# Performance work log

Hardware: AMD Instinct MI355X
Metric: run time of the kernel (lower is better)

The kernel has to match this reference:

```python
import jax, jax.numpy as jnp
import numpy as np


def setup_inputs() -> dict:
    key = jax.random.key(0)
    k1, k2 = jax.random.split(key)
    reconstructed_image = jax.random.normal(k1, (8, 1, 256, 256), dtype=jnp.float32)
    mask_embedding = jax.random.normal(k2, (8, 32, 256, 256), dtype=jnp.float32)
    return {"reconstructed_image": reconstructed_image, "mask_embedding": mask_embedding}


def reference(reconstructed_image, mask_embedding):
    # Original module: K = ortho-normalized 2D FFT of the real image;
    # for each k-space column i, zero all other columns, take ortho ifft2,
    # keep the real part -> separate_images[b, i, h, w].
    # By FFT linearity, ifft2 of a single-column k-space factorizes:
    #   ifft2(M_i * K)[h, w] = ifft_height(K[:, i])[h] * exp(2j*pi*w*i/W) / sqrt(W)
    # so we never materialize the (B, W, 2, H, W) masked k-space tensor.
    img = reconstructed_image[:, 0]                      # (B, H, W) real
    B, H, W = img.shape
    K = jnp.fft.fft2(img, norm='ortho')                  # (B, H, W) complex64
    col = jnp.fft.ifft(K, axis=1, norm='ortho')          # ifft along height: col[b, h, i]
    w_idx = jnp.arange(W)
    # phase[i, w] = exp(2j*pi*i*w/W) / sqrt(W)  (analytic width-basis)
    phase = (jnp.exp(2j * jnp.pi * jnp.outer(w_idx, w_idx) / W) / np.float32(np.sqrt(W))).astype(jnp.complex64)
    # separate_images[b, i, h, w] = Re(col[b, h, i] * phase[i, w])
    sep = jnp.einsum('bhi,iw->bihw', col, phase).real.astype(reconstructed_image.dtype)
    return jnp.concatenate([sep, mask_embedding], axis=1)  # (B, W+E, H, W)
```

## Files before the change

kernel.cpp:

```cpp
#include <hip/hip_runtime.h>


#define TWO_PI_OVER_256 0.02454369260617026f

typedef float vfloat4 __attribute__((ext_vector_type(4)));

__global__ __launch_bounds__(256) void dft_rows_kernel(const float* __restrict__ img,
                                                       float2* __restrict__ Ct) {
    __shared__ float row[256];
    const int t  = threadIdx.x;
    const int bh = blockIdx.x;
    row[t] = img[(size_t)bh * 256 + t];

    float ci, si;
    __sincosf((float)t * TWO_PI_OVER_256, &si, &ci);
    __syncthreads();

    float re = 0.f, im = 0.f;
    for (int xo = 0; xo < 256; xo += 32) {
        const int k = (t * xo) & 255;
        float c, s;
        __sincosf((float)k * TWO_PI_OVER_256, &s, &c);
#pragma unroll
        for (int x2 = 0; x2 < 32; ++x2) {
            const float r = row[xo + x2];
            re = fmaf(r, c, re);
            im = fmaf(r, s, im);
            const float cn = fmaf(c, ci, -s * si);
            s = fmaf(s, ci, c * si);
            c = cn;
        }
    }
    const int b = bh >> 8;
    const int h = bh & 255;
    Ct[((size_t)(b * 256 + t)) * 256 + h] =
        make_float2(re * (1.f / 256.f), im * (-1.f / 256.f));
}

__global__ __launch_bounds__(256) void expand_kernel(const float2* __restrict__ Ct,
                                                     float* __restrict__ out) {
    const int t   = threadIdx.x;
    const int blk = blockIdx.x;
    const int b   = blk >> 8;
    const int i   = blk & 255;

    __shared__ float2 cp[256];
    cp[t] = Ct[(size_t)blk * 256 + t];

    const int wb = (t & 63) * 4;
    float cw[4], sw[4];
#pragma unroll
    for (int j = 0; j < 4; ++j) {
        const int k = (i * (wb + j)) & 255;
        __sincosf((float)k * TWO_PI_OVER_256, &sw[j], &cw[j]);
    }
    __syncthreads();

    const int hl = t >> 6;
    float* __restrict__ obase = out + ((size_t)b * 288 + i) * 65536;
#pragma unroll 4
    for (int it = 0; it < 64; ++it) {
        const int h = it * 4 + hl;
        const float2 cv = cp[h];
        vfloat4 v;
        v.x = cv.x * cw[0] - cv.y * sw[0];
        v.y = cv.x * cw[1] - cv.y * sw[1];
        v.z = cv.x * cw[2] - cv.y * sw[2];
        v.w = cv.x * cw[3] - cv.y * sw[3];
        __builtin_nontemporal_store(v, reinterpret_cast<vfloat4*>(obase + (size_t)h * 256 + wb));
    }
}

__global__ __launch_bounds__(256) void mask_copy_kernel(const vfloat4* __restrict__ m,
                                                        vfloat4* __restrict__ out) {
    const size_t e = (size_t)blockIdx.x * 256 + threadIdx.x;
    const size_t b = e >> 19;
    const size_t r = e & 524287;
    const vfloat4 v = __builtin_nontemporal_load(&m[b * 524288 + r]);
    __builtin_nontemporal_store(v, &out[b * 4718592 + 4194304 + r]);
}

extern "C" void kernel_launch(void* const* d_in, const int* in_sizes, int n_in,
                              void* d_out, int out_size, void* d_ws, size_t ws_size,
                              hipStream_t stream) {
    const float* img  = (const float*)d_in[0];
    const float* mask = (const float*)d_in[1];
    float* out = (float*)d_out;

    float2* Ct = (float2*)(out + (size_t)256 * 65536);

    dft_rows_kernel<<<2048, 256, 0, stream>>>(img, Ct);
    expand_kernel<<<2048, 256, 0, stream>>>(Ct, out);
    mask_copy_kernel<<<16384, 256, 0, stream>>>((const vfloat4*)mask, (vfloat4*)out);
}
```

Measured before the change: 650.8 us.

## Fuse row DFT, expansion and mask copy into one kernel

Merges the three launches into a single kernel. Blocks past 2048 copy the mask embedding, eight vectors per thread. The other blocks compute, for their column i, the row DFT of each image row tile in shared memory, reduced with lane shuffles, and then write the expanded outputs directly. This removes the intermediate Ct buffer round trip and two launches, but each of the 256 blocks per batch now recomputes its own column's DFT over the whole image, reading it repeatedly from cache.

```diff
diff --git a/kernel.cpp b/kernel.cpp
--- a/kernel.cpp
+++ b/kernel.cpp
@@ -2,82 +2,95 @@
 
 
 #define TWO_PI_OVER_256 0.02454369260617026f
+#define SR 260
 
 typedef float vfloat4 __attribute__((ext_vector_type(4)));
 
-__global__ __launch_bounds__(256) void dft_rows_kernel(const float* __restrict__ img,
-                                                       float2* __restrict__ Ct) {
-    __shared__ float row[256];
-    const int t  = threadIdx.x;
-    const int bh = blockIdx.x;
-    row[t] = img[(size_t)bh * 256 + t];
-
-    float ci, si;
-    __sincosf((float)t * TWO_PI_OVER_256, &si, &ci);
-    __syncthreads();
-
-    float re = 0.f, im = 0.f;
-    for (int xo = 0; xo < 256; xo += 32) {
-        const int k = (t * xo) & 255;
-        float c, s;
-        __sincosf((float)k * TWO_PI_OVER_256, &s, &c);
-#pragma unroll
-        for (int x2 = 0; x2 < 32; ++x2) {
-            const float r = row[xo + x2];
-            re = fmaf(r, c, re);
-            im = fmaf(r, s, im);
-            const float cn = fmaf(c, ci, -s * si);
-            s = fmaf(s, ci, c * si);
-            c = cn;
-        }
-    }
-    const int b = bh >> 8;
-    const int h = bh & 255;
-    Ct[((size_t)(b * 256 + t)) * 256 + h] =
-        make_float2(re * (1.f / 256.f), im * (-1.f / 256.f));
-}
-
-__global__ __launch_bounds__(256) void expand_kernel(const float2* __restrict__ Ct,
-                                                     float* __restrict__ out) {
+__global__ __launch_bounds__(256) void fused_kernel(const float* __restrict__ img,
+                                                    const vfloat4* __restrict__ mask,
+                                                    float* __restrict__ out) {
     const int t   = threadIdx.x;
     const int blk = blockIdx.x;
-    const int b   = blk >> 8;
-    const int i   = blk & 255;
 
-    __shared__ float2 cp[256];
-    cp[t] = Ct[(size_t)blk * 256 + t];
+    if (blk >= 2048) {
+        const int mb = blk - 2048;
+#pragma unroll
+        for (int k = 0; k < 8; ++k) {
+            const size_t e = (size_t)mb * 256 + t + (size_t)k * 524288;
+            const size_t b = e >> 19;
+            const size_t r = e & 524287;
+            const vfloat4 v = __builtin_nontemporal_load(&mask[b * 524288 + r]);
+            __builtin_nontemporal_store(v, (vfloat4*)out + b * 4718592 + 4194304 + r);
+        }
+        return;
+    }
 
-    const int wb = (t & 63) * 4;
+    __shared__ float  rows[32 * SR];
+    __shared__ float2 cp[32];
+    const int b = blk >> 8;
+    const int i = blk & 255;
+
+    const int xc = t & 7;
+    const int hl = t >> 3;
+    float c0, s0, cst, sst;
+    __sincosf((float)((i * xc) & 255) * TWO_PI_OVER_256, &s0, &c0);
+    __sincosf((float)((i * 8)  & 255) * TWO_PI_OVER_256, &sst, &cst);
+
+    const int wb  = (t & 63) * 4;
+    const int hl2 = t >> 6;
     float cw[4], sw[4];
 #pragma unroll
     for (int j = 0; j < 4; ++j) {
         const int k = (i * (wb + j)) & 255;
         __sincosf((float)k * TWO_PI_OVER_256, &sw[j], &cw[j]);
     }
-    __syncthreads();
 
-    const int hl = t >> 6;
-    float* __restrict__ obase = out + ((size_t)b * 288 + i) * 65536;
-#pragma unroll 4
-    for (int it = 0; it < 64; ++it) {
-        const int h = it * 4 + hl;
-        const float2 cv = cp[h];
-        vfloat4 v;
-        v.x = cv.x * cw[0] - cv.y * sw[0];
-        v.y = cv.x * cw[1] - cv.y * sw[1];
-        v.z = cv.x * cw[2] - cv.y * sw[2];
-        v.w = cv.x * cw[3] - cv.y * sw[3];
-        __builtin_nontemporal_store(v, reinterpret_cast<vfloat4*>(obase + (size_t)h * 256 + wb));
+    const float* __restrict__ imgb  = img + (size_t)b * 65536;
+    float* __restrict__       obase = out + ((size_t)b * 288 + i) * 65536;
+
+    for (int tile = 0; tile < 8; ++tile) {
+        const int h0 = tile * 32;
+        const float2* __restrict__ src = (const float2*)(imgb + h0 * 256);
+#pragma unroll
+        for (int j = 0; j < 8; ++j) {
+            const int idx = t + j * 256;
+            const int rr  = idx >> 7;
+            const int c2  = idx & 127;
+            *(float2*)&rows[rr * SR + 2 * c2]        = src[rr * 128 + c2];
+            *(float2*)&rows[(rr + 16) * SR + 2 * c2] = src[(rr + 16) * 128 + c2];
+        }
+        __syncthreads();
+
+        float re = 0.f, im = 0.f, c = c0, s = s0;
+        const float* __restrict__ rp = &rows[hl * SR + xc];
+#pragma unroll
+        for (int x2 = 0; x2 < 32; ++x2) {
+            const float rv = rp[8 * x2];
+            re = fmaf(rv, c, re);
+            im = fmaf(rv, s, im);
+            const float cn = fmaf(c, cst, -s * sst);
+            s = fmaf(s, cst, c * sst);
+            c = cn;
+        }
+        re += __shfl_xor(re, 1); im += __shfl_xor(im, 1);
+        re += __shfl_xor(re, 2); im += __shfl_xor(im, 2);
+        re += __shfl_xor(re, 4); im += __shfl_xor(im, 4);
+        if (xc == 0) cp[hl] = make_float2(re * (1.f / 256.f), im * (-1.f / 256.f));
+        __syncthreads();
+
+#pragma unroll
+        for (int it2 = 0; it2 < 8; ++it2) {
+            const int h = it2 * 4 + hl2;
+            const float2 cv = cp[h];
+            vfloat4 v;
+            v.x = cv.x * cw[0] - cv.y * sw[0];
+            v.y = cv.x * cw[1] - cv.y * sw[1];
+            v.z = cv.x * cw[2] - cv.y * sw[2];
+            v.w = cv.x * cw[3] - cv.y * sw[3];
+            __builtin_nontemporal_store(
+                v, reinterpret_cast<vfloat4*>(obase + (size_t)(h0 + h) * 256 + wb));
+        }
     }
-}
-
-__global__ __launch_bounds__(256) void mask_copy_kernel(const vfloat4* __restrict__ m,
-                                                        vfloat4* __restrict__ out) {
-    const size_t e = (size_t)blockIdx.x * 256 + threadIdx.x;
-    const size_t b = e >> 19;
-    const size_t r = e & 524287;
-    const vfloat4 v = __builtin_nontemporal_load(&m[b * 524288 + r]);
-    __builtin_nontemporal_store(v, &out[b * 4718592 + 4194304 + r]);
 }
 
 extern "C" void kernel_launch(void* const* d_in, const int* in_sizes, int n_in,
@@ -87,9 +100,5 @@
     const float* mask = (const float*)d_in[1];
     float* out = (float*)d_out;
 
-    float2* Ct = (float2*)(out + (size_t)256 * 65536);
-
-    dft_rows_kernel<<<2048, 256, 0, stream>>>(img, Ct);
-    expand_kernel<<<2048, 256, 0, stream>>>(Ct, out);
-    mask_copy_kernel<<<16384, 256, 0, stream>>>((const vfloat4*)mask, (vfloat4*)out);
+    fused_kernel<<<4096, 256, 0, stream>>>(img, (const vfloat4*)mask, out);
 }
```

New measurement: 649.9 us, median of 2. About the same (-0.1%).
